# Performance work log

Hardware: AMD Instinct MI355X
Metric: run time of the kernel (lower is better)

## Reference

```python
import jax, jax.numpy as jnp
import numpy as np

EPS = 1e-5

def _mlp(x, w1, b1, w2, b2):
    # torch: Linear -> ReLU -> Linear (weights stored as (in, out))
    return jax.nn.relu(x @ w1 + b1) @ w2 + b2

def _ln(x, g, b):
    mu = x.mean(-1, keepdims=True)
    var = ((x - mu) ** 2).mean(-1, keepdims=True)
    return (x - mu) * jax.lax.rsqrt(var + EPS) * g + b

def setup_inputs():
    key = jax.random.key(0)
    B, N, d, d_out, M, K = 8, 8192, 256, 512, 2048, 16
    ks = jax.random.split(key, 16)
    def nrm(k, shape, s=0.05):
        return jax.random.normal(k, shape, jnp.float32) * s
    return dict(
        pos=jax.random.normal(ks[0], (B, N, 3), jnp.float32),
        feat=jax.random.normal(ks[1], (B, N, d), jnp.float32),
        fps_idx=jax.random.randint(ks[2], (B, M), 0, N, jnp.int32),
        knn_idx=jax.random.randint(ks[3], (B, M, K), 0, N, jnp.int32),
        cs1=16, cs2=64,
        mlp1_w1=nrm(ks[4], (2, 4, d), 0.3), mlp1_b1=jnp.zeros((2, d)),
        mlp1_w2=nrm(ks[5], (2, d, d)), mlp1_b2=jnp.zeros((2, d)),
        mlp2_w1=nrm(ks[6], (2, 6, d), 0.3), mlp2_b1=jnp.zeros((2, d)),
        mlp2_w2=nrm(ks[7], (2, d, d)), mlp2_b2=jnp.zeros((2, d)),
        wq=nrm(ks[8], (2, d, d)), wk=nrm(ks[9], (2, d, d)),
        wv=nrm(ks[10], (2, d, d)), wo=nrm(ks[11], (2, d, d)), bo=jnp.zeros((2, d)),
        ln_g=jnp.ones((2, d)), ln_b=jnp.zeros((2, d)),
        td_w=nrm(ks[12], (d, d_out)), td_b=jnp.zeros((d_out,)),
        bn_g=jnp.ones((d_out,)), bn_b=jnp.zeros((d_out,)),
        bn_mean=jnp.zeros((d_out,)), bn_var=jnp.ones((d_out,)),
    )

def reference(pos, feat, fps_idx, knn_idx, cs1, cs2,
              mlp1_w1, mlp1_b1, mlp1_w2, mlp1_b2,
              mlp2_w1, mlp2_b1, mlp2_w2, mlp2_b2,
              wq, wk, wv, wo, bo, ln_g, ln_b,
              td_w, td_b, bn_g, bn_b, bn_mean, bn_var):
    def block(f_in, cs, i):
        # DLPTBlock with equal-size contiguous clusters of size cs.
        # Note: original forward returns ln1(h_pos + dlsa_out); the ff branch is dead code.
        B, N, d = f_in.shape
        nc = N // cs
        pc = pos.reshape(B, nc, cs, 3)
        fc = f_in.reshape(B, nc, cs, d)
        cog = pc.mean(axis=2, keepdims=True)         # per-cluster center of gravity
        lp = pc - cog                                # local coords
        nrm = jnp.linalg.norm(lp, axis=-1, keepdims=True)
        h_pos = fc + _mlp(jnp.concatenate([lp, nrm], -1),
                          mlp1_w1[i], mlp1_b1[i], mlp1_w2[i], mlp1_b2[i])
        avg = jnp.broadcast_to(lp.mean(axis=2, keepdims=True), lp.shape)
        h_geo = fc + _mlp(jnp.concatenate([avg, lp], -1),
                          mlp2_w1[i], mlp2_b1[i], mlp2_w2[i], mlp2_b2[i])
        q = (h_geo @ wq[i]) / jnp.sqrt(jnp.float32(d))
        k = h_geo @ wk[i]
        v = h_pos @ wv[i]
        a = jax.nn.softmax(jnp.einsum('bcqd,bckd->bcqk', q, k), axis=-1)
        out = jnp.einsum('bcqk,bckd->bcqd', a, v) @ wo[i] + bo[i]
        return _ln(h_pos + out, ln_g[i], ln_b[i]).reshape(B, N, d)

    f = block(feat, cs1, 0)
    f = block(f, cs2, 1)
    # TransitionDown: linear -> BN (eval, running stats) -> relu -> knn max-pool
    f = f @ td_w + td_b
    f = jax.nn.relu((f - bn_mean) * jax.lax.rsqrt(bn_var + EPS) * bn_g + bn_b)
    pos_ds = jnp.take_along_axis(pos, fps_idx[..., None], axis=1)   # (B, M, 3)
    B = f.shape[0]
    f_knn = f[jnp.arange(B)[:, None, None], knn_idx]                # (B, M, K, d_out)
    feat_ds = f_knn.max(axis=2)
    return (pos_ds, feat_ds)
```

## Files before the change

### kernel.cpp

```cpp
#include <hip/hip_runtime.h>
#include <stdint.h>
#include <stddef.h>

typedef __attribute__((ext_vector_type(8))) short bf16x8;
typedef __attribute__((ext_vector_type(4))) float f32x4;
typedef __attribute__((ext_vector_type(8))) unsigned short u16x8;
typedef __attribute__((ext_vector_type(4))) unsigned short u16x4;
typedef __attribute__((ext_vector_type(2))) unsigned short u16x2;

#define DEVINL __device__ __forceinline__

DEVINL unsigned short f2b(float x){
  union { float f; unsigned int u; } v; v.f = x;
  return (unsigned short)((v.u + 0x7FFFu + ((v.u >> 16) & 1u)) >> 16);
}
DEVINL float b2f(unsigned short h){
  union { float f; unsigned int u; } v; v.u = ((unsigned int)h) << 16;
  return v.f;
}

DEVINL void gl_lds16(void* g, void* lds){
  __builtin_amdgcn_global_load_lds(
      (__attribute__((address_space(1))) void*)g,
      (__attribute__((address_space(3))) void*)lds, 16, 0, 0);
}

__global__ __launch_bounds__(256) void prep_k(
    const float* __restrict__ m1w2, const float* __restrict__ m2w2,
    const float* __restrict__ wqp,  const float* __restrict__ wkp,
    const float* __restrict__ wvp,  const float* __restrict__ wop,
    const float* __restrict__ tdw,  const float* __restrict__ tdb,
    const float* __restrict__ bng,  const float* __restrict__ bnb,
    const float* __restrict__ bnm,  const float* __restrict__ bnv,
    unsigned short* __restrict__ wT, float* __restrict__ bns, float* __restrict__ bnt)
{
  int idx = blockIdx.x * 256 + threadIdx.x;
  if (idx < 786432){
    int mat = idx >> 17;
    int e   = idx & 131071;
    int i   = e >> 16;
    int eb  = e & 65535;
    int n = eb >> 8, kx = eb & 255;
    const float* src; float sc = 1.0f;
    if      (mat == 0) src = m1w2;
    else if (mat == 1) src = m2w2;
    else if (mat == 2){ src = wqp; sc = 0.0625f; }
    else if (mat == 3) src = wkp;
    else if (mat == 4) src = wvp;
    else               src = wop;
    wT[idx] = f2b(src[i*65536 + kx*256 + n] * sc);
  } else if (idx < 917504){
    int e = idx - 786432;
    int n = e >> 8, kx = e & 255;
    wT[786432 + e] = f2b(tdw[kx*512 + n]);
  } else if (idx < 918016){
    int c = idx - 917504;
    float s = bng[c] * rsqrtf(bnv[c] + 1e-5f);
    bns[c] = s;
    bnt[c] = (tdb[c] - bnm[c]) * s + bnb[c];
  }
}

__global__ __launch_bounds__(256) void gemm_k(
    const unsigned short* __restrict__ A,
    const unsigned short* __restrict__ Wt,
    unsigned short* __restrict__ out,
    const float* __restrict__ bias,
    const unsigned short* __restrict__ addend,
    const float* __restrict__ bn_s,
    const float* __restrict__ bn_t,
    int ldc)
{
  __shared__ __attribute__((aligned(16))) unsigned short aT[512*8];
  __shared__ __attribute__((aligned(16))) unsigned short bT[512*8];
  __shared__ __attribute__((aligned(16))) unsigned short epi[128*140];

  const int tid  = threadIdx.x;
  const int lane = tid & 63;
  const int wave = tid >> 6;
  const int lrow = lane & 15, lq = lane >> 4;
  const int wr = wave >> 1, wc = wave & 1;
  const int m0 = blockIdx.x * 128;
  const int n0 = blockIdx.y * 128;

  f32x4 acc[4][4] = {};

  int aOff[4], bOff[4];
#pragma unroll
  for (int mt = 0; mt < 4; mt++){
    int row = wr*64 + mt*16 + lrow;
    aOff[mt] = row*64 + ((lq ^ ((row >> 1) & 3)) << 4);
  }
#pragma unroll
  for (int nt = 0; nt < 4; nt++){
    int row = wc*64 + nt*16 + lrow;
    bOff[nt] = row*64 + ((lq ^ ((row >> 1) & 3)) << 4);
  }

  const int s0 = tid, s1 = tid + 256;
  const int r0 = s0 >> 2, kc0 = (s0 & 3) ^ ((r0 >> 1) & 3);
  const int r1 = s1 >> 2, kc1 = (s1 & 3) ^ ((r1 >> 1) & 3);
  const unsigned short* Ab = A  + (size_t)m0 * 256;
  const unsigned short* Bb = Wt + (size_t)n0 * 256;
  char* aL = (char*)aT;
  char* bL = (char*)bT;
  const int wslot = wave * 64 * 16;

  for (int k0 = 0; k0 < 256; k0 += 32){
    __syncthreads();
    gl_lds16((void*)(Ab + r0*256 + k0 + kc0*8), aL + wslot);
    gl_lds16((void*)(Ab + r1*256 + k0 + kc1*8), aL + 4096 + wslot);
    gl_lds16((void*)(Bb + r0*256 + k0 + kc0*8), bL + wslot);
    gl_lds16((void*)(Bb + r1*256 + k0 + kc1*8), bL + 4096 + wslot);
    __syncthreads();
    bf16x8 af[4], bfr[4];
#pragma unroll
    for (int mt = 0; mt < 4; mt++) af[mt]  = *(const bf16x8*)(aL + aOff[mt]);
#pragma unroll
    for (int nt = 0; nt < 4; nt++) bfr[nt] = *(const bf16x8*)(bL + bOff[nt]);
#pragma unroll
    for (int mt = 0; mt < 4; mt++)
#pragma unroll
      for (int nt = 0; nt < 4; nt++)
        acc[mt][nt] = __builtin_amdgcn_mfma_f32_16x16x32_bf16(af[mt], bfr[nt], acc[mt][nt], 0, 0, 0);
  }

  __syncthreads();
#pragma unroll
  for (int mt = 0; mt < 4; mt++){
    int row = wr*64 + mt*16 + lq*4;
#pragma unroll
    for (int nt = 0; nt < 4; nt++){
      int col = wc*64 + nt*16 + lrow;
#pragma unroll
      for (int r = 0; r < 4; r++)
        epi[(row + r)*140 + col] = f2b(acc[mt][nt][r]);
    }
  }
  __syncthreads();

  const int erow = tid >> 1, h = tid & 1;
  const size_t gbase = (size_t)(m0 + erow) * (size_t)ldc + n0;
#pragma unroll
  for (int i = 0; i < 8; i++){
    int col = h*64 + i*8;
    u16x4 lo = *(const u16x4*)(&epi[erow*140 + col]);
    u16x4 hi = *(const u16x4*)(&epi[erow*140 + col + 4]);
    float y[8];
#pragma unroll
    for (int j = 0; j < 4; j++){ y[j] = b2f(lo[j]); y[4+j] = b2f(hi[j]); }
    if (addend){
      u16x8 ad = *(const u16x8*)(addend + gbase + col);
#pragma unroll
      for (int j = 0; j < 8; j++) y[j] += b2f(ad[j]);
    }
    if (bias){
#pragma unroll
      for (int j = 0; j < 8; j++) y[j] += bias[n0 + col + j];
    }
    if (bn_s){
#pragma unroll
      for (int j = 0; j < 8; j++){
        float t2 = y[j]*bn_s[n0 + col + j] + bn_t[n0 + col + j];
        y[j] = fmaxf(t2, 0.f);
      }
    }
    u16x8 o;
#pragma unroll
    for (int j = 0; j < 8; j++) o[j] = f2b(y[j]);
    *(u16x8*)(out + gbase + col) = o;
  }
}

DEVINL void wg_gemm1(const unsigned short* __restrict__ Wt,
                     const char* Als, int tid, f32x4 (&acc)[4])
{
  const int lane = tid & 63;
  const int wave = tid >> 6;
  const int lrow = lane & 15, lq = lane >> 4;
  const unsigned short* base = Wt + (size_t)(wave*16 + lrow)*256 + lq*8;

  bf16x8 bn = *(const bf16x8*)(base);
#pragma unroll
  for (int k = 0; k < 8; k++){
    bf16x8 b = bn;
    if (k < 7) bn = *(const bf16x8*)(base + (k+1)*32);
#pragma unroll
    for (int mt = 0; mt < 4; mt++){
      int row = mt*16 + lrow;
      bf16x8 af = *(const bf16x8*)(Als + row*512 + ((k*64 + lq*16) ^ ((row & 7) << 4)));
      acc[mt] = __builtin_amdgcn_mfma_f32_16x16x32_bf16(af, b, acc[mt], 0, 0, 0);
    }
  }
}

DEVINL void wg_epi_fc1(f32x4 (&acc)[4], char* Yls, const float* __restrict__ bias,
                       const unsigned int (&fcp)[4][2], int tid)
{
  const int lane = tid & 63, wave = tid >> 6;
  const int lrow = lane & 15, lq = lane >> 4;
  const int col = wave*16 + lrow;
  const float bv = bias[col];
#pragma unroll
  for (int mt = 0; mt < 4; mt++){
#pragma unroll
    for (int p = 0; p < 2; p++){
      unsigned int f = fcp[mt][p];
      int row0 = mt*16 + lq*4 + 2*p;
      int row1 = row0 + 1;
      float y0 = acc[mt][2*p]   + bv + b2f((unsigned short)f);
      float y1 = acc[mt][2*p+1] + bv + b2f((unsigned short)(f >> 16));
      *(unsigned short*)(Yls + row0*512 + ((col*2) ^ ((row0 & 7) << 4))) = f2b(y0);
      *(unsigned short*)(Yls + row1*512 + ((col*2) ^ ((row1 & 7) << 4))) = f2b(y1);
    }
  }
}

DEVINL void wg_epi_regs1(f32x4 (&acc)[4], const float* __restrict__ bias,
                         const unsigned int (&fcp)[4][2], unsigned int (&hp)[4][2],
                         int tid)
{
  const int lane = tid & 63, wave = tid >> 6;
  const int lrow = lane & 15;
  const int col = wave*16 + lrow;
  const float bv = bias[col];
#pragma unroll
  for (int mt = 0; mt < 4; mt++){
#pragma unroll
    for (int p = 0; p < 2; p++){
      unsigned int f = fcp[mt][p];
      float y0 = acc[mt][2*p]   + bv + b2f((unsigned short)f);
      float y1 = acc[mt][2*p+1] + bv + b2f((unsigned short)(f >> 16));
      hp[mt][p] = (unsigned int)f2b(y0) | ((unsigned int)f2b(y1) << 16);
    }
  }
}

DEVINL void wg_epi_plain1(f32x4 (&acc)[4], char* Yls, int tid)
{
  const int lane = tid & 63, wave = tid >> 6;
  const int lrow = lane & 15, lq = lane >> 4;
  const int col = wave*16 + lrow;
#pragma unroll
  for (int mt = 0; mt < 4; mt++){
#pragma unroll
    for (int r = 0; r < 4; r++){
      const int row = mt*16 + lq*4 + r;
      *(unsigned short*)(Yls + row*512 + ((col*2) ^ ((row & 7) << 4))) = f2b(acc[mt][r]);
    }
  }
}

DEVINL void wg_epi_vt1(f32x4 (&acc)[4], char* VT, int tid)
{
  const int lane = tid & 63, wave = tid >> 6;
  const int lrow = lane & 15, lq = lane >> 4;
  const int col = wave*16 + lrow;
#pragma unroll
  for (int mt = 0; mt < 4; mt++){
    const int row0 = mt*16 + lq*4;
    u16x4 w;
#pragma unroll
    for (int r = 0; r < 4; r++) w[r] = f2b(acc[mt][r]);
    *(u16x4*)(VT + col*128 + ((row0*2) ^ ((col & 7) << 4))) = w;
  }
}

template<int CS, bool F32IN>
__global__ __launch_bounds__(1024, 4) void block_k(
    const float* __restrict__ pos,
    const float* __restrict__ featF,
    const unsigned short* __restrict__ featB,
    const float* __restrict__ w1a, const float* __restrict__ b1a,
    const float* __restrict__ w1b, const float* __restrict__ b1b,
    const unsigned short* __restrict__ m1w2T, const float* __restrict__ m1b2,
    const unsigned short* __restrict__ m2w2T, const float* __restrict__ m2b2,
    const unsigned short* __restrict__ wqT, const unsigned short* __restrict__ wkT,
    const unsigned short* __restrict__ wvT, const unsigned short* __restrict__ woT,
    const float* __restrict__ bo, const float* __restrict__ lgam,
    const float* __restrict__ lbet,
    unsigned short* __restrict__ out)
{
  __shared__ __attribute__((aligned(16))) char smem[82240];
  char* BA = smem;
  char* BB = smem + 32768;
  char* Pm = smem + 65536;
  float (*P3)[3]    = (float(*)[3])(smem + 73728);
  float (*Cg)[3]    = (float(*)[3])(smem + 74496);
  float (*Gg)[4]    = (float(*)[4])(smem + 74560);
  float (*smx)[4]   = (float(*)[4])(smem + 75584);
  float (*ssm)[4]   = (float(*)[4])(smem + 76608);
  float (*sred)[8]  = (float(*)[8])(smem + 77632);
  float (*s2red)[8] = (float(*)[8])(smem + 79680);
  float* mub = (float*)(smem + 81728);
  float* rsb = (float*)(smem + 81984);

  const int tid  = threadIdx.x;
  const int lane = tid & 63;
  const int wave = tid >> 6;
  const int lrow = lane & 15, lq = lane >> 4;
  const int m0 = blockIdx.x * 64;

  unsigned short* gout = out + (size_t)m0 * 256;

  unsigned int fcp[4][2];
  {
    const int col = wave*16 + lrow;
    if constexpr (F32IN){
      const float* resF = featF + (size_t)m0 * 256;
#pragma unroll
      for (int mt = 0; mt < 4; mt++)
#pragma unroll
        for (int p = 0; p < 2; p++){
          int row0 = mt*16 + lq*4 + 2*p;
          unsigned int lo = f2b(resF[row0*256 + col]);
          unsigned int hi = f2b(resF[(row0+1)*256 + col]);
          fcp[mt][p] = lo | (hi << 16);
        }
    } else {
      const unsigned short* resB = featB + (size_t)m0 * 256;
#pragma unroll
      for (int mt = 0; mt < 4; mt++)
#pragma unroll
        for (int p = 0; p < 2; p++){
          int row0 = mt*16 + lq*4 + 2*p;
          unsigned int lo = resB[row0*256 + col];
          unsigned int hi = resB[(row0+1)*256 + col];
          fcp[mt][p] = lo | (hi << 16);
        }
    }
  }

  if (tid < 64){
    P3[tid][0] = pos[(size_t)(m0+tid)*3 + 0];
    P3[tid][1] = pos[(size_t)(m0+tid)*3 + 1];
    P3[tid][2] = pos[(size_t)(m0+tid)*3 + 2];
  }
  __syncthreads();

  constexpr int NCH = 64 / CS;
  if (tid < NCH*3){
    int ch = tid / 3, c = tid - ch*3;
    float s = 0.f;
    for (int r = 0; r < CS; r++) s += P3[ch*CS + r][c];
    Cg[ch][c] = s / (float)CS;
  }
  __syncthreads();
  if (tid < 64){
    int ch = (CS == 16) ? (tid >> 4) : 0;
    float x = P3[tid][0] - Cg[ch][0];
    float y = P3[tid][1] - Cg[ch][1];
    float z = P3[tid][2] - Cg[ch][2];
    Gg[tid][0] = x; Gg[tid][1] = y; Gg[tid][2] = z;
    Gg[tid][3] = sqrtf(x*x + y*y + z*z);
  }
  __syncthreads();

  {
    const int c = tid & 255;
    const int r0 = (tid >> 8) * 16;
    const float wb0 = w1b[768+c], wb1 = w1b[1024+c], wb2 = w1b[1280+c];
    const float bb  = b1b[c];
    for (int r = r0; r < r0 + 16; r++){
      float v2 = bb + Gg[r][0]*wb0 + Gg[r][1]*wb1 + Gg[r][2]*wb2;
      *(unsigned short*)(BA + r*512 + ((c*2) ^ ((r & 7) << 4))) = f2b(fmaxf(v2, 0.f));
    }
  }
  __syncthreads();
  {
    f32x4 acc[4] = {};
    wg_gemm1(m2w2T, BA, tid, acc);
    wg_epi_fc1(acc, BB, m2b2, fcp, tid);
    __syncthreads();
  }
  {
    const int c = tid & 255;
    const int r0 = (tid >> 8) * 16;
    const float wa0 = w1a[c], wa1 = w1a[256+c], wa2 = w1a[512+c], wa3 = w1a[768+c];
    const float ba  = b1a[c];
    for (int r = r0; r < r0 + 16; r++){
      float v1 = ba + Gg[r][0]*wa0 + Gg[r][1]*wa1 + Gg[r][2]*wa2 + Gg[r][3]*wa3;
      *(unsigned short*)(BA + r*512 + ((c*2) ^ ((r & 7) << 4))) = f2b(fmaxf(v1, 0.f));
    }
  }
  __syncthreads();
  unsigned int hp[4][2];
  {
    f32x4 acc[4] = {};
    wg_gemm1(m1w2T, BA, tid, acc);
    wg_epi_regs1(acc, m1b2, fcp, hp, tid);
    __syncthreads();
  }
  {
    f32x4 acc[4] = {};
    wg_gemm1(wqT, BB, tid, acc);
    wg_epi_plain1(acc, BA, tid);
    __syncthreads();
  }
  {
    f32x4 acc[4] = {};
    wg_gemm1(wkT, BB, tid, acc);
    __syncthreads();
    wg_epi_plain1(acc, BB, tid);
    __syncthreads();
  }

  if (CS == 64){
    const int tr = wave & 3, tc = wave >> 2;
    f32x4 sacc = {};
    const int qrow = tr*16 + lrow;
    const int brow = tc*16 + lrow;
    const int qsw  = (qrow & 7) << 4;
    const int bsw  = (brow & 7) << 4;
#pragma unroll
    for (int kk = 0; kk < 8; kk++){
      bf16x8 aq = *(const bf16x8*)(BA + qrow*512 + ((kk*64 + lq*16) ^ qsw));
      bf16x8 bk = *(const bf16x8*)(BB + brow*512 + ((kk*64 + lq*16) ^ bsw));
      sacc = __builtin_amdgcn_mfma_f32_16x16x32_bf16(aq, bk, sacc, 0, 0, 0);
    }
#pragma unroll
    for (int r = 0; r < 4; r++){
      float m = sacc[r];
#pragma unroll
      for (int d = 1; d < 16; d <<= 1) m = fmaxf(m, __shfl_xor(m, d));
      float e = __expf(sacc[r] - m);
      sacc[r] = e;
      float s = e;
#pragma unroll
      for (int d = 1; d < 16; d <<= 1) s += __shfl_xor(s, d);
      if (lrow == 0){
        int row = tr*16 + lq*4 + r;
        smx[row][tc] = m;
        ssm[row][tc] = s;
      }
    }
    __syncthreads();
#pragma unroll
    for (int r = 0; r < 4; r++){
      int row = tr*16 + lq*4 + r;
      float m0v = smx[row][0], m1v = smx[row][1], m2v = smx[row][2], m3v = smx[row][3];
      float M = fmaxf(fmaxf(m0v, m1v), fmaxf(m2v, m3v));
      float S = ssm[row][0]*__expf(m0v - M) + ssm[row][1]*__expf(m1v - M)
              + ssm[row][2]*__expf(m2v - M) + ssm[row][3]*__expf(m3v - M);
      float f = __expf(smx[row][tc] - M) / S;
      int col = tc*16 + lrow;
      *(unsigned short*)(Pm + row*128 + ((col*2) ^ ((row & 7) << 4))) = f2b(sacc[r]*f);
    }
    __syncthreads();
  } else {
    if (wave < 4){
      f32x4 sacc = {};
      const int qrow = wave*16 + lrow;
      const int qsw  = (qrow & 7) << 4;
#pragma unroll
      for (int kk = 0; kk < 8; kk++){
        bf16x8 aq = *(const bf16x8*)(BA + qrow*512 + ((kk*64 + lq*16) ^ qsw));
        bf16x8 bk = *(const bf16x8*)(BB + qrow*512 + ((kk*64 + lq*16) ^ qsw));
        sacc = __builtin_amdgcn_mfma_f32_16x16x32_bf16(aq, bk, sacc, 0, 0, 0);
      }
#pragma unroll
      for (int r = 0; r < 4; r++){
        float m = sacc[r];
#pragma unroll
        for (int d = 1; d < 16; d <<= 1) m = fmaxf(m, __shfl_xor(m, d));
        float e = __expf(sacc[r] - m);
        float s = e;
#pragma unroll
        for (int d = 1; d < 16; d <<= 1) s += __shfl_xor(s, d);
        int row = wave*16 + lq*4 + r;
        *(unsigned short*)(Pm + row*64 + ((lrow*2) ^ ((row & 3) << 4))) = f2b(e / s);
      }
    } else if (tid < 512){
      int t2 = tid - 256;
      int row = t2 >> 2, j = t2 & 3;
      u16x4 z = {};
      *(u16x4*)(Pm + row*64 + ((32 + j*8) ^ ((row & 3) << 4))) = z;
    }
    __syncthreads();
  }

  {
    const int col = wave*16 + lrow;
#pragma unroll
    for (int mt = 0; mt < 4; mt++)
#pragma unroll
      for (int p = 0; p < 2; p++){
        int row0 = mt*16 + lq*4 + 2*p;
        int row1 = row0 + 1;
        unsigned int d = hp[mt][p];
        *(unsigned short*)(BA + row0*512 + ((col*2) ^ ((row0 & 7) << 4))) = (unsigned short)d;
        *(unsigned short*)(BA + row1*512 + ((col*2) ^ ((row1 & 7) << 4))) = (unsigned short)(d >> 16);
      }
  }
  __syncthreads();
  {
    f32x4 acc[4] = {};
    wg_gemm1(wvT, BA, tid, acc);
    wg_epi_vt1(acc, BB, tid);
    __syncthreads();
  }

  {
    f32x4 oacc[4] = {};
    const int d = wave*16 + lrow;
    const int dsw = (d & 7) << 4;
    if (CS == 64){
#pragma unroll
      for (int kk = 0; kk < 2; kk++){
        bf16x8 bv = *(const bf16x8*)(BB + d*128 + ((kk*64 + lq*16) ^ dsw));
#pragma unroll
        for (int mt = 0; mt < 4; mt++){
          int row = mt*16 + lrow;
          bf16x8 ap = *(const bf16x8*)(Pm + row*128 + ((kk*64 + lq*16) ^ ((row & 7) << 4)));
          oacc[mt] = __builtin_amdgcn_mfma_f32_16x16x32_bf16(ap, bv, oacc[mt], 0, 0, 0);
        }
      }
    } else {
#pragma unroll
      for (int mt = 0; mt < 4; mt++){
        int row = mt*16 + lrow;
        bf16x8 ap = *(const bf16x8*)(Pm + row*64 + ((lq*16) ^ ((row & 3) << 4)));
        bf16x8 bv = *(const bf16x8*)(BB + d*128 + ((mt*32 + (lq & 1)*16) ^ dsw));
        oacc[mt] = __builtin_amdgcn_mfma_f32_16x16x32_bf16(ap, bv, oacc[mt], 0, 0, 0);
      }
    }
#pragma unroll
    for (int mt = 0; mt < 4; mt++){
#pragma unroll
      for (int r = 0; r < 4; r++){
        int row = mt*16 + lq*4 + r;
        *(unsigned short*)(BA + row*512 + ((d*2) ^ ((row & 7) << 4))) = f2b(oacc[mt][r]);
      }
    }
    __syncthreads();
  }

  {
    f32x4 yacc[4] = {};
    wg_gemm1(woT, BA, tid, yacc);
    __syncthreads();
    const int col = wave*16 + lrow;
    const float bov = bo[col];
#pragma unroll
    for (int mt = 0; mt < 4; mt++){
#pragma unroll
      for (int p = 0; p < 2; p++){
        int row0 = mt*16 + lq*4 + 2*p;
        int row1 = row0 + 1;
        unsigned int d = hp[mt][p];
        float z0 = yacc[mt][2*p]   + bov + b2f((unsigned short)d);
        float z1 = yacc[mt][2*p+1] + bov + b2f((unsigned short)(d >> 16));
        *(unsigned short*)(BA + row0*512 + ((col*2) ^ ((row0 & 7) << 4))) = f2b(z0);
        *(unsigned short*)(BA + row1*512 + ((col*2) ^ ((row1 & 7) << 4))) = f2b(z1);
      }
    }
    __syncthreads();
  }
  {
    const int row = (tid >> 3) & 63, part = tid & 7;
    const size_t gr = (size_t)row * 256;
    const int sw = (row & 7) << 4;
    if (tid < 512){
      float sm = 0.f, sq = 0.f;
#pragma unroll
      for (int i = 0; i < 4; i++){
        int col = part*32 + i*8;
        u16x8 v = *(const u16x8*)(BA + row*512 + ((col*2) ^ sw));
#pragma unroll
        for (int j = 0; j < 8; j++){
          float y = b2f(v[j]);
          sm += y; sq += y*y;
        }
      }
      sred[row][part] = sm; s2red[row][part] = sq;
    }
    __syncthreads();
    if (tid < 64){
      float s = 0.f, q2 = 0.f;
#pragma unroll
      for (int p = 0; p < 8; p++){ s += sred[tid][p]; q2 += s2red[tid][p]; }
      float mu = s * (1.0f/256.0f);
      float var = q2 * (1.0f/256.0f) - mu*mu;
      mub[tid] = mu;
      rsb[tid] = rsqrtf(var + 1e-5f);
    }
    __syncthreads();
    if (tid < 512){
      const float mu = mub[row], rs = rsb[row];
#pragma unroll
      for (int i = 0; i < 4; i++){
        int col = part*32 + i*8;
        u16x8 v = *(const u16x8*)(BA + row*512 + ((col*2) ^ sw));
        u16x8 o;
#pragma unroll
        for (int j = 0; j < 8; j++)
          o[j] = f2b((b2f(v[j]) - mu)*rs*lgam[col + j] + lbet[col + j]);
        *(u16x8*)(gout + gr + col) = o;
      }
    }
  }
}

__global__ __launch_bounds__(256) void out_k(
    const unsigned short* __restrict__ F2,
    const float* __restrict__ pos,
    const int* __restrict__ fps,
    const int* __restrict__ knn,
    float* __restrict__ outp)
{
  const int p = blockIdx.x * 4 + (threadIdx.x >> 6);
  const int t = threadIdx.x & 63;
  const int b = p >> 11;
  const int* kn = knn + (size_t)p * 16;
  const int c = t * 8;
  const unsigned short* Fb = F2 + (size_t)b * 8192 * 512 + c;

  float m[8];
#pragma unroll
  for (int q = 0; q < 8; q++) m[q] = -3.0e38f;
#pragma unroll
  for (int j = 0; j < 16; j++){
    int idx = kn[j];
    u16x8 v = *(const u16x8*)(Fb + (size_t)idx * 512);
#pragma unroll
    for (int q = 0; q < 8; q++) m[q] = fmaxf(m[q], b2f(v[q]));
  }
  float* of = outp + 49152 + (size_t)p * 512 + c;
  float4 o0, o1;
  o0.x = m[0]; o0.y = m[1]; o0.z = m[2]; o0.w = m[3];
  o1.x = m[4]; o1.y = m[5]; o1.z = m[6]; o1.w = m[7];
  *(float4*)of = o0;
  *(float4*)(of + 4) = o1;
  if (t < 3){
    int fi = fps[p];
    outp[(size_t)p*3 + t] = pos[((size_t)b*8192 + fi)*3 + t];
  }
}

extern "C" void kernel_launch(void* const* d_in, const int* in_sizes, int n_in,
                              void* d_out, int out_size, void* d_ws, size_t ws_size,
                              hipStream_t stream)
{
  (void)in_sizes; (void)n_in; (void)out_size; (void)ws_size;

  const float* pos  = (const float*)d_in[0];
  const float* feat = (const float*)d_in[1];
  const int*   fps  = (const int*)d_in[2];
  const int*   knn  = (const int*)d_in[3];
  const float* m1w1 = (const float*)d_in[6];
  const float* m1b1 = (const float*)d_in[7];
  const float* m1w2 = (const float*)d_in[8];
  const float* m1b2 = (const float*)d_in[9];
  const float* m2w1 = (const float*)d_in[10];
  const float* m2b1 = (const float*)d_in[11];
  const float* m2w2 = (const float*)d_in[12];
  const float* m2b2 = (const float*)d_in[13];
  const float* wq   = (const float*)d_in[14];
  const float* wk   = (const float*)d_in[15];
  const float* wv   = (const float*)d_in[16];
  const float* wo   = (const float*)d_in[17];
  const float* bo   = (const float*)d_in[18];
  const float* lng  = (const float*)d_in[19];
  const float* lnb  = (const float*)d_in[20];
  const float* tdw  = (const float*)d_in[21];
  const float* tdb  = (const float*)d_in[22];
  const float* bng  = (const float*)d_in[23];
  const float* bnb  = (const float*)d_in[24];
  const float* bnm  = (const float*)d_in[25];
  const float* bnv  = (const float*)d_in[26];

  char* ws = (char*)d_ws;
  unsigned short* wT = (unsigned short*)ws;
  float* bns = (float*)(ws + 1835008);
  float* bnt = (float*)(ws + 1837056);
  const size_t SLOT = 33554432;
  unsigned short* A  = (unsigned short*)(ws + 2097152);
  unsigned short* Bs = (unsigned short*)(ws + 2097152 + SLOT);
  unsigned short* E  = (unsigned short*)(ws + 2097152 + 2*SLOT);

  auto wtm = [&](int mat, int i){ return wT + (size_t)mat*131072 + (size_t)i*65536; };
  unsigned short* tdT = wT + 786432;

  prep_k<<<3586, 256, 0, stream>>>(m1w2, m2w2, wq, wk, wv, wo, tdw, tdb, bng, bnb, bnm, bnv,
                                   wT, bns, bnt);

  block_k<16, true><<<1024, 1024, 0, stream>>>(
      pos, feat, nullptr,
      m1w1, m1b1, m2w1, m2b1,
      wtm(0,0), m1b2, wtm(1,0), m2b2,
      wtm(2,0), wtm(3,0), wtm(4,0), wtm(5,0),
      bo, lng, lnb, A);

  block_k<64, false><<<1024, 1024, 0, stream>>>(
      pos, nullptr, A,
      m1w1 + 1024, m1b1 + 256, m2w1 + 1536, m2b1 + 256,
      wtm(0,1), m1b2 + 256, wtm(1,1), m2b2 + 256,
      wtm(2,1), wtm(3,1), wtm(4,1), wtm(5,1),
      bo + 256, lng + 256, lnb + 256, Bs);

  gemm_k<<<dim3(512,4), 256, 0, stream>>>(Bs, tdT, E, nullptr, nullptr, bns, bnt, 512);

  out_k<<<4096, 256, 0, stream>>>(E, pos, fps, knn, (float*)d_out);
}
```

Baseline: 570.1 us.

## Add third LDS buffer to pair GEMMs and cut block-level barriers

Adds a third 32KB shared-memory staging buffer so the two MLP second-layer GEMMs and the Q/K projections can run back-to-back without intermediate barriers, and reassigns buffers for V, attention output and the pre-LayerNorm sum to remove several __syncthreads. It also switches float-to-bf16 conversion to the native __bf16 cast when available. The larger LDS footprint (about 115KB per block of 1024 threads) may limit how many blocks fit per CU.

```diff
diff --git a/kernel.cpp b/kernel.cpp
--- a/kernel.cpp
+++ b/kernel.cpp
@@ -10,10 +10,18 @@
 
 #define DEVINL __device__ __forceinline__
 
+#if defined(__BF16_MANT_DIG__)
+DEVINL unsigned short f2b(float x){
+  union { __bf16 b; unsigned short u; } v;
+  v.b = (__bf16)x;
+  return v.u;
+}
+#else
 DEVINL unsigned short f2b(float x){
   union { float f; unsigned int u; } v; v.f = x;
   return (unsigned short)((v.u + 0x7FFFu + ((v.u >> 16) & 1u)) >> 16);
 }
+#endif
 DEVINL float b2f(unsigned short h){
   union { float f; unsigned int u; } v; v.u = ((unsigned int)h) << 16;
   return v.f;
@@ -281,19 +289,20 @@
     const float* __restrict__ lbet,
     unsigned short* __restrict__ out)
 {
-  __shared__ __attribute__((aligned(16))) char smem[82240];
+  __shared__ __attribute__((aligned(16))) char smem[115008];
   char* BA = smem;
   char* BB = smem + 32768;
-  char* Pm = smem + 65536;
-  float (*P3)[3]    = (float(*)[3])(smem + 73728);
-  float (*Cg)[3]    = (float(*)[3])(smem + 74496);
-  float (*Gg)[4]    = (float(*)[4])(smem + 74560);
-  float (*smx)[4]   = (float(*)[4])(smem + 75584);
-  float (*ssm)[4]   = (float(*)[4])(smem + 76608);
-  float (*sred)[8]  = (float(*)[8])(smem + 77632);
-  float (*s2red)[8] = (float(*)[8])(smem + 79680);
-  float* mub = (float*)(smem + 81728);
-  float* rsb = (float*)(smem + 81984);
+  char* BC = smem + 65536;
+  char* Pm = smem + 98304;
+  float (*P3)[3]    = (float(*)[3])(smem + 106496);
+  float (*Cg)[3]    = (float(*)[3])(smem + 107264);
+  float (*Gg)[4]    = (float(*)[4])(smem + 107328);
+  float (*smx)[4]   = (float(*)[4])(smem + 108352);
+  float (*ssm)[4]   = (float(*)[4])(smem + 109376);
+  float (*sred)[8]  = (float(*)[8])(smem + 110400);
+  float (*s2red)[8] = (float(*)[8])(smem + 112448);
+  float* mub = (float*)(smem + 114496);
+  float* rsb = (float*)(smem + 114752);
 
   const int tid  = threadIdx.x;
   const int lane = tid & 63;
@@ -361,50 +370,52 @@
     const int r0 = (tid >> 8) * 16;
     const float wb0 = w1b[768+c], wb1 = w1b[1024+c], wb2 = w1b[1280+c];
     const float bb  = b1b[c];
+    const float wa0 = w1a[c], wa1 = w1a[256+c], wa2 = w1a[512+c], wa3 = w1a[768+c];
+    const float ba  = b1a[c];
     for (int r = r0; r < r0 + 16; r++){
       float v2 = bb + Gg[r][0]*wb0 + Gg[r][1]*wb1 + Gg[r][2]*wb2;
-      *(unsigned short*)(BA + r*512 + ((c*2) ^ ((r & 7) << 4))) = f2b(fmaxf(v2, 0.f));
-    }
-  }
-  __syncthreads();
+      float v1 = ba + Gg[r][0]*wa0 + Gg[r][1]*wa1 + Gg[r][2]*wa2 + Gg[r][3]*wa3;
+      int off = ((c*2) ^ ((r & 7) << 4));
+      *(unsigned short*)(BA + r*512 + off) = f2b(fmaxf(v2, 0.f));
+      *(unsigned short*)(BC + r*512 + off) = f2b(fmaxf(v1, 0.f));
+    }
+  }
+  __syncthreads();
+
+  unsigned int hp[4][2];
   {
     f32x4 acc[4] = {};
     wg_gemm1(m2w2T, BA, tid, acc);
     wg_epi_fc1(acc, BB, m2b2, fcp, tid);
-    __syncthreads();
-  }
-  {
-    const int c = tid & 255;
-    const int r0 = (tid >> 8) * 16;
-    const float wa0 = w1a[c], wa1 = w1a[256+c], wa2 = w1a[512+c], wa3 = w1a[768+c];
-    const float ba  = b1a[c];
-    for (int r = r0; r < r0 + 16; r++){
-      float v1 = ba + Gg[r][0]*wa0 + Gg[r][1]*wa1 + Gg[r][2]*wa2 + Gg[r][3]*wa3;
-      *(unsigned short*)(BA + r*512 + ((c*2) ^ ((r & 7) << 4))) = f2b(fmaxf(v1, 0.f));
-    }
-  }
-  __syncthreads();
-  unsigned int hp[4][2];
-  {
-    f32x4 acc[4] = {};
-    wg_gemm1(m1w2T, BA, tid, acc);
-    wg_epi_regs1(acc, m1b2, fcp, hp, tid);
-    __syncthreads();
-  }
+    f32x4 acc2[4] = {};
+    wg_gemm1(m1w2T, BC, tid, acc2);
+    wg_epi_regs1(acc2, m1b2, fcp, hp, tid);
+  }
+  __syncthreads();
+
   {
     f32x4 acc[4] = {};
     wg_gemm1(wqT, BB, tid, acc);
     wg_epi_plain1(acc, BA, tid);
-    __syncthreads();
-  }
-  {
-    f32x4 acc[4] = {};
-    wg_gemm1(wkT, BB, tid, acc);
-    __syncthreads();
-    wg_epi_plain1(acc, BB, tid);
-    __syncthreads();
-  }
-
+    f32x4 acc2[4] = {};
+    wg_gemm1(wkT, BB, tid, acc2);
+    wg_epi_plain1(acc2, BC, tid);
+  }
+  __syncthreads();
+
+  {
+    const int col = wave*16 + lrow;
+#pragma unroll
+    for (int mt = 0; mt < 4; mt++)
+#pragma unroll
+      for (int p = 0; p < 2; p++){
+        int row0 = mt*16 + lq*4 + 2*p;
+        int row1 = row0 + 1;
+        unsigned int d = hp[mt][p];
+        *(unsigned short*)(BB + row0*512 + ((col*2) ^ ((row0 & 7) << 4))) = (unsigned short)d;
+        *(unsigned short*)(BB + row1*512 + ((col*2) ^ ((row1 & 7) << 4))) = (unsigned short)(d >> 16);
+      }
+  }
   if (CS == 64){
     const int tr = wave & 3, tc = wave >> 2;
     f32x4 sacc = {};
@@ -415,7 +426,7 @@
 #pragma unroll
     for (int kk = 0; kk < 8; kk++){
       bf16x8 aq = *(const bf16x8*)(BA + qrow*512 + ((kk*64 + lq*16) ^ qsw));
-      bf16x8 bk = *(const bf16x8*)(BB + brow*512 + ((kk*64 + lq*16) ^ bsw));
+      bf16x8 bk = *(const bf16x8*)(BC + brow*512 + ((kk*64 + lq*16) ^ bsw));
       sacc = __builtin_amdgcn_mfma_f32_16x16x32_bf16(aq, bk, sacc, 0, 0, 0);
     }
 #pragma unroll
@@ -455,7 +466,7 @@
 #pragma unroll
       for (int kk = 0; kk < 8; kk++){
         bf16x8 aq = *(const bf16x8*)(BA + qrow*512 + ((kk*64 + lq*16) ^ qsw));
-        bf16x8 bk = *(const bf16x8*)(BB + qrow*512 + ((kk*64 + lq*16) ^ qsw));
+        bf16x8 bk = *(const bf16x8*)(BC + qrow*512 + ((kk*64 + lq*16) ^ qsw));
         sacc = __builtin_amdgcn_mfma_f32_16x16x32_bf16(aq, bk, sacc, 0, 0, 0);
       }
 #pragma unroll
@@ -480,25 +491,11 @@
   }
 
   {
-    const int col = wave*16 + lrow;
-#pragma unroll
-    for (int mt = 0; mt < 4; mt++)
-#pragma unroll
-      for (int p = 0; p < 2; p++){
-        int row0 = mt*16 + lq*4 + 2*p;
-        int row1 = row0 + 1;
-        unsigned int d = hp[mt][p];
-        *(unsigned short*)(BA + row0*512 + ((col*2) ^ ((row0 & 7) << 4))) = (unsigned short)d;
-        *(unsigned short*)(BA + row1*512 + ((col*2) ^ ((row1 & 7) << 4))) = (unsigned short)(d >> 16);
-      }
-  }
-  __syncthreads();
-  {
     f32x4 acc[4] = {};
-    wg_gemm1(wvT, BA, tid, acc);
-    wg_epi_vt1(acc, BB, tid);
-    __syncthreads();
-  }
+    wg_gemm1(wvT, BB, tid, acc);
+    wg_epi_vt1(acc, BA, tid);
+  }
+  __syncthreads();
 
   {
     f32x4 oacc[4] = {};
@@ -507,7 +504,7 @@
     if (CS == 64){
 #pragma unroll
       for (int kk = 0; kk < 2; kk++){
-        bf16x8 bv = *(const bf16x8*)(BB + d*128 + ((kk*64 + lq*16) ^ dsw));
+        bf16x8 bv = *(const bf16x8*)(BA + d*128 + ((kk*64 + lq*16) ^ dsw));
 #pragma unroll
         for (int mt = 0; mt < 4; mt++){
           int row = mt*16 + lrow;
@@ -520,7 +517,7 @@
       for (int mt = 0; mt < 4; mt++){
         int row = mt*16 + lrow;
         bf16x8 ap = *(const bf16x8*)(Pm + row*64 + ((lq*16) ^ ((row & 3) << 4)));
-        bf16x8 bv = *(const bf16x8*)(BB + d*128 + ((mt*32 + (lq & 1)*16) ^ dsw));
+        bf16x8 bv = *(const bf16x8*)(BA + d*128 + ((mt*32 + (lq & 1)*16) ^ dsw));
         oacc[mt] = __builtin_amdgcn_mfma_f32_16x16x32_bf16(ap, bv, oacc[mt], 0, 0, 0);
       }
     }
@@ -529,16 +526,15 @@
 #pragma unroll
       for (int r = 0; r < 4; r++){
         int row = mt*16 + lq*4 + r;
-        *(unsigned short*)(BA + row*512 + ((d*2) ^ ((row & 7) << 4))) = f2b(oacc[mt][r]);
-      }
-    }
-    __syncthreads();
-  }
+        *(unsigned short*)(BC + row*512 + ((d*2) ^ ((row & 7) << 4))) = f2b(oacc[mt][r]);
+      }
+    }
+  }
+  __syncthreads();
 
   {
     f32x4 yacc[4] = {};
-    wg_gemm1(woT, BA, tid, yacc);
-    __syncthreads();
+    wg_gemm1(woT, BC, tid, yacc);
     const int col = wave*16 + lrow;
     const float bov = bo[col];
 #pragma unroll
@@ -550,12 +546,13 @@
         unsigned int d = hp[mt][p];
         float z0 = yacc[mt][2*p]   + bov + b2f((unsigned short)d);
         float z1 = yacc[mt][2*p+1] + bov + b2f((unsigned short)(d >> 16));
-        *(unsigned short*)(BA + row0*512 + ((col*2) ^ ((row0 & 7) << 4))) = f2b(z0);
-        *(unsigned short*)(BA + row1*512 + ((col*2) ^ ((row1 & 7) << 4))) = f2b(z1);
-      }
-    }
-    __syncthreads();
-  }
+        *(unsigned short*)(BB + row0*512 + ((col*2) ^ ((row0 & 7) << 4))) = f2b(z0);
+        *(unsigned short*)(BB + row1*512 + ((col*2) ^ ((row1 & 7) << 4))) = f2b(z1);
+      }
+    }
+  }
+  __syncthreads();
+
   {
     const int row = (tid >> 3) & 63, part = tid & 7;
     const size_t gr = (size_t)row * 256;
@@ -565,7 +562,7 @@
 #pragma unroll
       for (int i = 0; i < 4; i++){
         int col = part*32 + i*8;
-        u16x8 v = *(const u16x8*)(BA + row*512 + ((col*2) ^ sw));
+        u16x8 v = *(const u16x8*)(BB + row*512 + ((col*2) ^ sw));
 #pragma unroll
         for (int j = 0; j < 8; j++){
           float y = b2f(v[j]);
@@ -590,7 +587,7 @@
 #pragma unroll
       for (int i = 0; i < 4; i++){
         int col = part*32 + i*8;
-        u16x8 v = *(const u16x8*)(BA + row*512 + ((col*2) ^ sw));
+        u16x8 v = *(const u16x8*)(BB + row*512 + ((col*2) ^ sw));
         u16x8 o;
 #pragma unroll
         for (int j = 0; j < 8; j++)
```

Result: no change. 581.2 us (+1.9%).
